# Kernel optimization log

Measured on AMD Instinct MI355X. Metric: run time of the kernel, lower is better.

## Reference

```python
import jax, jax.numpy as jnp
import numpy as np

N_NODES = 100000
N_EDGES = 1600000
N_FEAT = 128
HIDDEN = 128
N_GRAPHS = 1024


def setup_inputs() -> dict:
    key = jax.random.key(0)
    ks = jax.random.split(key, 9)
    x = jax.random.normal(ks[0], (N_NODES, N_FEAT), dtype=jnp.float32)
    edge_index = jax.random.randint(ks[1], (2, N_EDGES), 0, N_NODES, dtype=jnp.int64)
    batch = jnp.sort(jax.random.randint(ks[2], (N_NODES,), 0, N_GRAPHS, dtype=jnp.int64))
    W1 = jax.random.normal(ks[3], (N_FEAT, HIDDEN), dtype=jnp.float32) * (1.0 / np.sqrt(N_FEAT))
    b1 = jax.random.normal(ks[4], (HIDDEN,), dtype=jnp.float32) * 0.01
    W2 = jax.random.normal(ks[5], (HIDDEN, HIDDEN), dtype=jnp.float32) * (1.0 / np.sqrt(HIDDEN))
    b2 = jax.random.normal(ks[6], (HIDDEN,), dtype=jnp.float32) * 0.01
    Wl = jax.random.normal(ks[7], (HIDDEN, 2), dtype=jnp.float32) * (1.0 / np.sqrt(HIDDEN))
    bl = jax.random.normal(ks[8], (2,), dtype=jnp.float32) * 0.01
    return {"x": x, "edge_index": edge_index, "batch": batch,
            "W1": W1, "b1": b1, "W2": W2, "b2": b2, "Wl": Wl, "bl": bl}


def _gcn_norm(edge_index, num_nodes):
    # PyG GCNConv: add self-loops, then sym-normalize with in-degree (target col).
    loop = jnp.arange(num_nodes, dtype=edge_index.dtype)
    src = jnp.concatenate([edge_index[0], loop])  # [E+N]
    dst = jnp.concatenate([edge_index[1], loop])  # [E+N]
    deg = jax.ops.segment_sum(jnp.ones_like(dst, dtype=jnp.float32), dst,
                              num_segments=num_nodes)
    dinv = jnp.where(deg > 0, jax.lax.rsqrt(deg), 0.0)
    norm = dinv[src] * dinv[dst]  # [E+N]
    return src, dst, norm


def _gcn_conv(h, W, b, src, dst, norm, num_nodes):
    h = h @ W                                   # [N, out]
    msg = h[src] * norm[:, None]                # gather + scale, [E+N, out]
    agg = jax.ops.segment_sum(msg, dst, num_segments=num_nodes)  # scatter-add
    return agg + b


def reference(x, edge_index, batch, W1, b1, W2, b2, Wl, bl):
    n = x.shape[0]
    src, dst, norm = _gcn_norm(edge_index, n)
    h = jax.nn.relu(_gcn_conv(x, W1, b1, src, dst, norm, n))
    h = jax.nn.relu(_gcn_conv(h, W2, b2, src, dst, norm, n))
    # global_mean_pool over graph ids
    sums = jax.ops.segment_sum(h, batch, num_segments=N_GRAPHS)        # [G, H]
    counts = jax.ops.segment_sum(jnp.ones((n,), jnp.float32), batch,
                                 num_segments=N_GRAPHS)
    pooled = sums / jnp.maximum(counts, 1.0)[:, None]
    # F.dropout with training=False default in inference -> identity
    return pooled @ Wl + bl  # [G, 2]
```

## Files before the change

### kernel.cpp

```cpp
#include <hip/hip_runtime.h>
#include <hip/hip_bf16.h>

#define N_NODES 100000
#define N_EDGES 1600000
#define FEAT 128
#define N_GRAPHS 1024
#define NBUCK 391
#define CHUNK 4096

typedef short short8 __attribute__((ext_vector_type(8)));
typedef float float4v __attribute__((ext_vector_type(4)));

static __device__ inline unsigned short f2bf(float f) {
    __hip_bfloat16 b = __float2bfloat16(f);
    unsigned short r;
    __builtin_memcpy(&r, &b, 2);
    return r;
}
static __device__ inline float bf_lo(unsigned int v) { return __uint_as_float(v << 16); }
static __device__ inline float bf_hi(unsigned int v) { return __uint_as_float(v & 0xFFFF0000u); }

__global__ __launch_bounds__(256) void k_hist(const int* __restrict__ dst,
                                              int* __restrict__ bcount) {
    __shared__ int h[NBUCK];
    for (int i = threadIdx.x; i < NBUCK; i += 256) h[i] = 0;
    __syncthreads();
    for (int e = blockIdx.x * 256 + threadIdx.x; e < N_EDGES; e += gridDim.x * 256)
        atomicAdd(&h[dst[e] >> 8], 1);
    __syncthreads();
    for (int i = threadIdx.x; i < NBUCK; i += 256) {
        int c = h[i];
        if (c) atomicAdd(&bcount[i], c);
    }
}

__global__ __launch_bounds__(512) void k_scan391(const int* __restrict__ in,
                                                 int* __restrict__ base,
                                                 int* __restrict__ cur,
                                                 int* __restrict__ tail) {
    int t = threadIdx.x;
    int v = (t < NBUCK) ? in[t] : 0;
    int lane = t & 63, wid = t >> 6;
    int s = v;
#pragma unroll
    for (int d = 1; d < 64; d <<= 1) { int n = __shfl_up(s, d); if (lane >= d) s += n; }
    __shared__ int ws[8];
    if (lane == 63) ws[wid] = s;
    __syncthreads();
    if (t < 8) {
        int x = ws[t];
#pragma unroll
        for (int d = 1; d < 8; d <<= 1) { int n = __shfl_up(x, d); if ((int)t >= d) x += n; }
        ws[t] = x;
    }
    __syncthreads();
    int excl = s - v + (wid ? ws[wid - 1] : 0);
    if (t < NBUCK) {
        base[t] = excl;
        if (cur) cur[t] = excl;
    }
    if (t == 0 && tail) tail[0] = N_EDGES;
}

__global__ __launch_bounds__(256) void k_bucket(const int* __restrict__ src,
                                                const int* __restrict__ dst,
                                                int* __restrict__ bcur,
                                                uint2* __restrict__ pairs) {
    __shared__ int cnt[NBUCK];
    __shared__ int basebuf[NBUCK];
    int t = threadIdx.x;
    int e0 = blockIdx.x * CHUNK;
    for (int i = t; i < NBUCK; i += 256) cnt[i] = 0;
    __syncthreads();
    int es[16], ed[16];
#pragma unroll
    for (int j = 0; j < 16; ++j) {
        int e = e0 + j * 256 + t;
        if (e < N_EDGES) {
            es[j] = src[e];
            ed[j] = dst[e];
            atomicAdd(&cnt[ed[j] >> 8], 1);
        } else ed[j] = -1;
    }
    __syncthreads();
    for (int i = t; i < NBUCK; i += 256) {
        int c = cnt[i];
        basebuf[i] = c ? atomicAdd(&bcur[i], c) : 0;
        cnt[i] = 0;
    }
    __syncthreads();
#pragma unroll
    for (int j = 0; j < 16; ++j) {
        if (ed[j] >= 0) {
            int b = ed[j] >> 8;
            int p = basebuf[b] + atomicAdd(&cnt[b], 1);
            pairs[p] = make_uint2((unsigned)es[j], (unsigned)ed[j]);
        }
    }
}

__global__ __launch_bounds__(256) void k_bdeg(const uint2* __restrict__ pairs,
                                              const int* __restrict__ bbase,
                                              const int* __restrict__ bcount,
                                              int* __restrict__ deg,
                                              float* __restrict__ dinv,
                                              int* __restrict__ wsum) {
    __shared__ int d[256];
    __shared__ int wr[4];
    int b = blockIdx.x, t = threadIdx.x;
    d[t] = 0;
    __syncthreads();
    int s0 = bbase[b], n = bcount[b];
    for (int i = t; i < n; i += 256) atomicAdd(&d[pairs[s0 + i].y & 255], 1);
    __syncthreads();
    int node = b * 256 + t;
    int v = d[t];
    if (node < N_NODES) {
        deg[node] = v;
        dinv[node] = rsqrtf((float)(v + 1));
    }
#pragma unroll
    for (int dd = 32; dd > 0; dd >>= 1) v += __shfl_down(v, dd);
    if ((t & 63) == 0) wr[t >> 6] = v;
    __syncthreads();
    if (t == 0) wsum[b] = wr[0] + wr[1] + wr[2] + wr[3];
}

__global__ __launch_bounds__(256) void k_bfill(const uint2* __restrict__ pairs,
                                               const int* __restrict__ bbase,
                                               const int* __restrict__ bcount,
                                               const int* __restrict__ deg,
                                               const int* __restrict__ wbase,
                                               int* __restrict__ offs,
                                               int* __restrict__ csr) {
    __shared__ int lcur[256];
    __shared__ int ws[4];
    int b = blockIdx.x, t = threadIdx.x;
    int node = b * 256 + t;
    int dv = (node < N_NODES) ? deg[node] : 0;
    int lane = t & 63, wid = t >> 6;
    int s = dv;
#pragma unroll
    for (int d = 1; d < 64; d <<= 1) { int n = __shfl_up(s, d); if (lane >= d) s += n; }
    if (lane == 63) ws[wid] = s;
    __syncthreads();
    if (t < 4) {
        int x = ws[t];
#pragma unroll
        for (int d = 1; d < 4; d <<= 1) { int n = __shfl_up(x, d); if ((int)t >= d) x += n; }
        ws[t] = x;
    }
    __syncthreads();
    int excl = s - dv + (wid ? ws[wid - 1] : 0) + wbase[b];
    if (node < N_NODES) offs[node] = excl;
    lcur[t] = excl;
    __syncthreads();
    int s0 = bbase[b], n = bcount[b];
    for (int i = t; i < n; i += 256) {
        uint2 pr = pairs[s0 + i];
        int p = atomicAdd(&lcur[pr.y & 255], 1);
        csr[p] = (int)pr.x;
    }
}

__global__ __launch_bounds__(256) void k_prepW(const float* __restrict__ W,
                                               unsigned short* __restrict__ wp) {
    int t = blockIdx.x * 256 + threadIdx.x;
    if (t >= 16384) return;
    int k = t >> 7, n = t & 127;
    float w = W[k * 128 + n];
    unsigned ub = __float_as_uint(w);
    unsigned short hi = (unsigned short)(ub >> 16);
    float hif = __uint_as_float(ub & 0xFFFF0000u);
    unsigned short lo = f2bf(w - hif);
    int sidx = n * 128 + ((k & 7) | (8 * (((k >> 3) ^ n) & 15)));
    wp[sidx] = hi;
    wp[16384 + sidx] = lo;
}

__global__ __launch_bounds__(256) void k_gemm_mfma(const float* __restrict__ inp,
                                                   const unsigned short* __restrict__ wp,
                                                   const float* __restrict__ dinv,
                                                   unsigned short* __restrict__ u) {
    __shared__ unsigned short sW[32768];
    {
        float4* d4 = (float4*)sW;
        const float4* s4 = (const float4*)wp;
#pragma unroll
        for (int i = 0; i < 16; ++i) d4[threadIdx.x + 256 * i] = s4[threadIdx.x + 256 * i];
    }
    __syncthreads();
    const int t = threadIdx.x;
    const int wv = t >> 6, L = t & 63;
    const int m = L & 15, q = L >> 4;
    const int r0 = blockIdx.x * 64 + wv * 16;
    int arow = r0 + m;
    if (arow >= N_NODES) arow = N_NODES - 1;
    const float4* ap = (const float4*)(inp + (size_t)arow * 128);
    float4v acc[8];
#pragma unroll
    for (int c = 0; c < 8; ++c) acc[c] = (float4v){0.f, 0.f, 0.f, 0.f};

#pragma unroll
    for (int k0 = 0; k0 < 128; k0 += 32) {
        float4 f0 = ap[(k0 >> 2) + 2 * q];
        float4 f1 = ap[(k0 >> 2) + 2 * q + 1];
        float fa[8] = {f0.x, f0.y, f0.z, f0.w, f1.x, f1.y, f1.z, f1.w};
        short8 ah, al;
#pragma unroll
        for (int j = 0; j < 8; ++j) {
            unsigned ub = __float_as_uint(fa[j]);
            ah[j] = (short)(ub >> 16);
            float hif = __uint_as_float(ub & 0xFFFF0000u);
            al[j] = (short)f2bf(fa[j] - hif);
        }
        const int b = (k0 >> 3) + q;
#pragma unroll
        for (int c = 0; c < 8; ++c) {
            int ng = c * 16 + m;
            int elem = ng * 128 + 8 * ((b ^ ng) & 15);
            short8 bh = *(const short8*)&sW[elem];
            short8 bl = *(const short8*)&sW[16384 + elem];
            acc[c] = __builtin_amdgcn_mfma_f32_16x16x32_bf16(ah, bh, acc[c], 0, 0, 0);
            acc[c] = __builtin_amdgcn_mfma_f32_16x16x32_bf16(al, bh, acc[c], 0, 0, 0);
            acc[c] = __builtin_amdgcn_mfma_f32_16x16x32_bf16(ah, bl, acc[c], 0, 0, 0);
        }
    }
#pragma unroll
    for (int r = 0; r < 4; ++r) {
        int row = r0 + 4 * q + r;
        if (row < N_NODES) {
            float dv = dinv[row];
            unsigned short* up = u + (size_t)row * 128 + m;
#pragma unroll
            for (int c = 0; c < 8; ++c) up[c * 16] = f2bf(dv * acc[c][r]);
        }
    }
}

__global__ __launch_bounds__(256) void k_agg(const unsigned int* __restrict__ u,
                                             const int* __restrict__ offs,
                                             const int* __restrict__ csr,
                                             const float* __restrict__ dinv,
                                             const float* __restrict__ bias,
                                             float* __restrict__ hout) {
    int wid = threadIdx.x >> 6;
    int lane = threadIdx.x & 63;
    int node = __builtin_amdgcn_readfirstlane(blockIdx.x * 4 + wid);
    if (node >= N_NODES) return;
    int p = __builtin_amdgcn_readfirstlane(offs[node]);
    int e = __builtin_amdgcn_readfirstlane(offs[node + 1]);
    unsigned int self = u[(size_t)node * 64 + lane];
    float ax0 = bf_lo(self), ay0 = bf_hi(self);
    float ax1 = 0.f, ay1 = 0.f, ax2 = 0.f, ay2 = 0.f, ax3 = 0.f, ay3 = 0.f;
    float ax4 = 0.f, ay4 = 0.f, ax5 = 0.f, ay5 = 0.f, ax6 = 0.f, ay6 = 0.f;
    float ax7 = 0.f, ay7 = 0.f;
    for (; p < e; p += 8) {
        int c0 = csr[p + 0], c1 = csr[p + 1], c2 = csr[p + 2], c3 = csr[p + 3];
        int c4 = csr[p + 4], c5 = csr[p + 5], c6 = csr[p + 6], c7 = csr[p + 7];
        int i0 = c0;
        int i1 = (p + 1 < e) ? c1 : N_NODES;
        int i2 = (p + 2 < e) ? c2 : N_NODES;
        int i3 = (p + 3 < e) ? c3 : N_NODES;
        int i4 = (p + 4 < e) ? c4 : N_NODES;
        int i5 = (p + 5 < e) ? c5 : N_NODES;
        int i6 = (p + 6 < e) ? c6 : N_NODES;
        int i7 = (p + 7 < e) ? c7 : N_NODES;
        unsigned v0 = (u + (size_t)i0 * 64)[lane];
        unsigned v1 = (u + (size_t)i1 * 64)[lane];
        unsigned v2 = (u + (size_t)i2 * 64)[lane];
        unsigned v3 = (u + (size_t)i3 * 64)[lane];
        unsigned v4 = (u + (size_t)i4 * 64)[lane];
        unsigned v5 = (u + (size_t)i5 * 64)[lane];
        unsigned v6 = (u + (size_t)i6 * 64)[lane];
        unsigned v7 = (u + (size_t)i7 * 64)[lane];
        ax0 += bf_lo(v0); ay0 += bf_hi(v0);
        ax1 += bf_lo(v1); ay1 += bf_hi(v1);
        ax2 += bf_lo(v2); ay2 += bf_hi(v2);
        ax3 += bf_lo(v3); ay3 += bf_hi(v3);
        ax4 += bf_lo(v4); ay4 += bf_hi(v4);
        ax5 += bf_lo(v5); ay5 += bf_hi(v5);
        ax6 += bf_lo(v6); ay6 += bf_hi(v6);
        ax7 += bf_lo(v7); ay7 += bf_hi(v7);
    }
    float d = dinv[node];
    float2 b = ((const float2*)bias)[lane];
    float sx = ((ax0 + ax1) + (ax2 + ax3)) + ((ax4 + ax5) + (ax6 + ax7));
    float sy = ((ay0 + ay1) + (ay2 + ay3)) + ((ay4 + ay5) + (ay6 + ay7));
    float r0 = fmaxf(d * sx + b.x, 0.f);
    float r1 = fmaxf(d * sy + b.y, 0.f);
    ((float2*)hout)[(size_t)node * 64 + lane] = make_float2(r0, r1);
}

__global__ __launch_bounds__(128) void k_pool(const float* __restrict__ h,
                                              const int* __restrict__ batch,
                                              const float* __restrict__ Wl,
                                              const float* __restrict__ bl,
                                              float* __restrict__ out) {
    int g = blockIdx.x;
    int c = threadIdx.x;
    __shared__ int sb[2];
    if (c < 2) {
        int tgt = g + c;
        int lo = 0, hi = N_NODES;
        while (lo < hi) { int m = (lo + hi) >> 1; if (batch[m] < tgt) lo = m + 1; else hi = m; }
        sb[c] = lo;
    }
    __syncthreads();
    int s0 = sb[0], s1 = sb[1];
    float sum = 0.f;
    for (int i = s0; i < s1; ++i) sum += h[(size_t)i * 128 + c];
    float cnt = (float)(s1 - s0);
    float pooled = sum / fmaxf(cnt, 1.0f);
    __shared__ float red[128];
    float w0 = Wl[c * 2 + 0], w1 = Wl[c * 2 + 1];
    red[c] = pooled * w0;
    __syncthreads();
    for (int st = 64; st > 0; st >>= 1) { if (c < st) red[c] += red[c + st]; __syncthreads(); }
    if (c == 0) out[g * 2 + 0] = red[0] + bl[0];
    __syncthreads();
    red[c] = pooled * w1;
    __syncthreads();
    for (int st = 64; st > 0; st >>= 1) { if (c < st) red[c] += red[c + st]; __syncthreads(); }
    if (c == 0) out[g * 2 + 1] = red[0] + bl[1];
}

extern "C" void kernel_launch(void* const* d_in, const int* in_sizes, int n_in,
                              void* d_out, int out_size, void* d_ws, size_t ws_size,
                              hipStream_t stream) {
    const float* x  = (const float*)d_in[0];
    const int* ei   = (const int*)d_in[1];
    const int* batch = (const int*)d_in[2];
    const float* W1 = (const float*)d_in[3];
    const float* b1 = (const float*)d_in[4];
    const float* W2 = (const float*)d_in[5];
    const float* b2 = (const float*)d_in[6];
    const float* Wl = (const float*)d_in[7];
    const float* bl = (const float*)d_in[8];
    float* out = (float*)d_out;
    const int* src = ei;
    const int* dst = ei + N_EDGES;

    char* ws = (char*)d_ws;
    size_t o = 0;
    auto alloc = [&](size_t bytes) -> void* {
        o = (o + 255) & ~(size_t)255;
        void* p = ws + o;
        o += bytes;
        return p;
    };
    int* bcount = (int*)alloc((size_t)NBUCK * 4);
    int* bbase  = (int*)alloc((size_t)NBUCK * 4);
    int* bcur   = (int*)alloc((size_t)NBUCK * 4);
    int* wsum   = (int*)alloc((size_t)NBUCK * 4);
    int* wbase  = (int*)alloc((size_t)NBUCK * 4);
    int* deg    = (int*)alloc((size_t)N_NODES * 4);
    float* dinv = (float*)alloc((size_t)N_NODES * 4);
    int* offs   = (int*)alloc((size_t)(N_NODES + 1) * 4);
    unsigned short* wp1 = (unsigned short*)alloc(65536);
    unsigned short* wp2 = (unsigned short*)alloc(65536);
    uint2* pairs = (uint2*)alloc((size_t)N_EDGES * 8);
    int* csr    = (int*)alloc((size_t)(N_EDGES + 8) * 4);
    unsigned short* u = (unsigned short*)alloc((size_t)(N_NODES + 1) * 128 * 2);
    float* h    = (float*)alloc((size_t)N_NODES * 128 * 4);

    hipMemsetAsync(bcount, 0, (size_t)NBUCK * 4, stream);
    hipMemsetAsync(u + (size_t)N_NODES * 128, 0, 256, stream);
    k_prepW<<<64, 256, 0, stream>>>(W1, wp1);
    k_prepW<<<64, 256, 0, stream>>>(W2, wp2);
    k_hist<<<256, 256, 0, stream>>>(dst, bcount);
    k_scan391<<<1, 512, 0, stream>>>(bcount, bbase, bcur, nullptr);
    k_bucket<<<(N_EDGES + CHUNK - 1) / CHUNK, 256, 0, stream>>>(src, dst, bcur, pairs);
    k_bdeg<<<NBUCK, 256, 0, stream>>>(pairs, bbase, bcount, deg, dinv, wsum);
    k_scan391<<<1, 512, 0, stream>>>(wsum, wbase, nullptr, &offs[N_NODES]);
    k_bfill<<<NBUCK, 256, 0, stream>>>(pairs, bbase, bcount, deg, wbase, offs, csr);

    const int gemmGrid = (N_NODES + 63) / 64;
    k_gemm_mfma<<<gemmGrid, 256, 0, stream>>>(x, wp1, dinv, u);
    k_agg<<<(N_NODES + 3) / 4, 256, 0, stream>>>((const unsigned int*)u, offs, csr, dinv, b1, h);
    k_gemm_mfma<<<gemmGrid, 256, 0, stream>>>(h, wp2, dinv, u);
    k_agg<<<(N_NODES + 3) / 4, 256, 0, stream>>>((const unsigned int*)u, offs, csr, dinv, b2, h);

    k_pool<<<N_GRAPHS, 128, 0, stream>>>(h, batch, Wl, bl, out);
}
```

Before: 375.2 us.

## Store hidden activations as split bf16 hi/lo, pack edge pairs, fuse prep kernels

The aggregation kernel now writes its output as two bf16 planes (hi and residual lo) in place of fp32. A new GEMM variant feeds these planes straight into MFMA without converting fp32 to bf16 itself, and pooling sums hi+lo. Edge bucket pairs are packed into one 32-bit word (src<<8 | dst&255), halving that intermediate traffic. The two weight-prep kernels and the memsets are merged into one launch. Total bytes moved stay about the same for h, but the GEMM's conversion work and launch overhead go down. Packing src<<8 relies on node ids fitting in 24 bits.

```diff
diff --git a/kernel.cpp b/kernel.cpp
--- a/kernel.cpp
+++ b/kernel.cpp
@@ -19,6 +19,32 @@
 }
 static __device__ inline float bf_lo(unsigned int v) { return __uint_as_float(v << 16); }
 static __device__ inline float bf_hi(unsigned int v) { return __uint_as_float(v & 0xFFFF0000u); }
+static __device__ inline float bf_s(unsigned short s) { return __uint_as_float(((unsigned)s) << 16); }
+
+__global__ __launch_bounds__(256) void k_prep(const float* __restrict__ W1,
+                                              const float* __restrict__ W2,
+                                              unsigned short* __restrict__ wp1,
+                                              unsigned short* __restrict__ wp2,
+                                              int* __restrict__ bcount,
+                                              unsigned int* __restrict__ udummy) {
+    int bid = blockIdx.x;
+    const float* W = (bid < 64) ? W1 : W2;
+    unsigned short* wp = (bid < 64) ? wp1 : wp2;
+    int t = (bid & 63) * 256 + threadIdx.x;
+    int k = t >> 7, n = t & 127;
+    float w = W[k * 128 + n];
+    unsigned ub = __float_as_uint(w);
+    unsigned short hi = (unsigned short)(ub >> 16);
+    float hif = __uint_as_float(ub & 0xFFFF0000u);
+    unsigned short lo = f2bf(w - hif);
+    int sidx = n * 128 + ((k & 7) | (8 * (((k >> 3) ^ n) & 15)));
+    wp[sidx] = hi;
+    wp[16384 + sidx] = lo;
+    if (bid == 0) {
+        for (int i = threadIdx.x; i < NBUCK; i += 256) bcount[i] = 0;
+        if (threadIdx.x < 64) udummy[threadIdx.x] = 0;
+    }
+}
 
 __global__ __launch_bounds__(256) void k_hist(const int* __restrict__ dst,
                                               int* __restrict__ bcount) {
@@ -65,22 +91,23 @@
 __global__ __launch_bounds__(256) void k_bucket(const int* __restrict__ src,
                                                 const int* __restrict__ dst,
                                                 int* __restrict__ bcur,
-                                                uint2* __restrict__ pairs) {
+                                                unsigned int* __restrict__ pairs) {
     __shared__ int cnt[NBUCK];
     __shared__ int basebuf[NBUCK];
     int t = threadIdx.x;
     int e0 = blockIdx.x * CHUNK;
     for (int i = t; i < NBUCK; i += 256) cnt[i] = 0;
     __syncthreads();
-    int es[16], ed[16];
+    unsigned pk[16]; int bk[16];
 #pragma unroll
     for (int j = 0; j < 16; ++j) {
         int e = e0 + j * 256 + t;
         if (e < N_EDGES) {
-            es[j] = src[e];
-            ed[j] = dst[e];
-            atomicAdd(&cnt[ed[j] >> 8], 1);
-        } else ed[j] = -1;
+            int s = src[e], d = dst[e];
+            bk[j] = d >> 8;
+            pk[j] = ((unsigned)s << 8) | (unsigned)(d & 255);
+            atomicAdd(&cnt[bk[j]], 1);
+        } else bk[j] = -1;
     }
     __syncthreads();
     for (int i = t; i < NBUCK; i += 256) {
@@ -91,15 +118,14 @@
     __syncthreads();
 #pragma unroll
     for (int j = 0; j < 16; ++j) {
-        if (ed[j] >= 0) {
-            int b = ed[j] >> 8;
-            int p = basebuf[b] + atomicAdd(&cnt[b], 1);
-            pairs[p] = make_uint2((unsigned)es[j], (unsigned)ed[j]);
-        }
-    }
-}
-
-__global__ __launch_bounds__(256) void k_bdeg(const uint2* __restrict__ pairs,
+        if (bk[j] >= 0) {
+            int p = basebuf[bk[j]] + atomicAdd(&cnt[bk[j]], 1);
+            pairs[p] = pk[j];
+        }
+    }
+}
+
+__global__ __launch_bounds__(256) void k_bdeg(const unsigned int* __restrict__ pairs,
                                               const int* __restrict__ bbase,
                                               const int* __restrict__ bcount,
                                               int* __restrict__ deg,
@@ -111,7 +137,7 @@
     d[t] = 0;
     __syncthreads();
     int s0 = bbase[b], n = bcount[b];
-    for (int i = t; i < n; i += 256) atomicAdd(&d[pairs[s0 + i].y & 255], 1);
+    for (int i = t; i < n; i += 256) atomicAdd(&d[pairs[s0 + i] & 255u], 1);
     __syncthreads();
     int node = b * 256 + t;
     int v = d[t];
@@ -126,7 +152,7 @@
     if (t == 0) wsum[b] = wr[0] + wr[1] + wr[2] + wr[3];
 }
 
-__global__ __launch_bounds__(256) void k_bfill(const uint2* __restrict__ pairs,
+__global__ __launch_bounds__(256) void k_bfill(const unsigned int* __restrict__ pairs,
                                                const int* __restrict__ bbase,
                                                const int* __restrict__ bcount,
                                                const int* __restrict__ deg,
@@ -157,25 +183,10 @@
     __syncthreads();
     int s0 = bbase[b], n = bcount[b];
     for (int i = t; i < n; i += 256) {
-        uint2 pr = pairs[s0 + i];
-        int p = atomicAdd(&lcur[pr.y & 255], 1);
-        csr[p] = (int)pr.x;
-    }
-}
-
-__global__ __launch_bounds__(256) void k_prepW(const float* __restrict__ W,
-                                               unsigned short* __restrict__ wp) {
-    int t = blockIdx.x * 256 + threadIdx.x;
-    if (t >= 16384) return;
-    int k = t >> 7, n = t & 127;
-    float w = W[k * 128 + n];
-    unsigned ub = __float_as_uint(w);
-    unsigned short hi = (unsigned short)(ub >> 16);
-    float hif = __uint_as_float(ub & 0xFFFF0000u);
-    unsigned short lo = f2bf(w - hif);
-    int sidx = n * 128 + ((k & 7) | (8 * (((k >> 3) ^ n) & 15)));
-    wp[sidx] = hi;
-    wp[16384 + sidx] = lo;
+        unsigned pr = pairs[s0 + i];
+        int p = atomicAdd(&lcur[pr & 255u], 1);
+        csr[p] = (int)(pr >> 8);
+    }
 }
 
 __global__ __launch_bounds__(256) void k_gemm_mfma(const float* __restrict__ inp,
@@ -238,12 +249,66 @@
     }
 }
 
+__global__ __launch_bounds__(256) void k_gemm_mfma_bf(const unsigned short* __restrict__ hh,
+                                                      const unsigned short* __restrict__ hl,
+                                                      const unsigned short* __restrict__ wp,
+                                                      const float* __restrict__ dinv,
+                                                      unsigned short* __restrict__ u) {
+    __shared__ unsigned short sW[32768];
+    {
+        float4* d4 = (float4*)sW;
+        const float4* s4 = (const float4*)wp;
+#pragma unroll
+        for (int i = 0; i < 16; ++i) d4[threadIdx.x + 256 * i] = s4[threadIdx.x + 256 * i];
+    }
+    __syncthreads();
+    const int t = threadIdx.x;
+    const int wv = t >> 6, L = t & 63;
+    const int m = L & 15, q = L >> 4;
+    const int r0 = blockIdx.x * 64 + wv * 16;
+    int arow = r0 + m;
+    if (arow >= N_NODES) arow = N_NODES - 1;
+    const unsigned short* hhp = hh + (size_t)arow * 128 + 8 * q;
+    const unsigned short* hlp = hl + (size_t)arow * 128 + 8 * q;
+    float4v acc[8];
+#pragma unroll
+    for (int c = 0; c < 8; ++c) acc[c] = (float4v){0.f, 0.f, 0.f, 0.f};
+
+#pragma unroll
+    for (int k0 = 0; k0 < 128; k0 += 32) {
+        short8 ah = *(const short8*)(hhp + k0);
+        short8 al = *(const short8*)(hlp + k0);
+        const int b = (k0 >> 3) + q;
+#pragma unroll
+        for (int c = 0; c < 8; ++c) {
+            int ng = c * 16 + m;
+            int elem = ng * 128 + 8 * ((b ^ ng) & 15);
+            short8 bh = *(const short8*)&sW[elem];
+            short8 bl = *(const short8*)&sW[16384 + elem];
+            acc[c] = __builtin_amdgcn_mfma_f32_16x16x32_bf16(ah, bh, acc[c], 0, 0, 0);
+            acc[c] = __builtin_amdgcn_mfma_f32_16x16x32_bf16(al, bh, acc[c], 0, 0, 0);
+            acc[c] = __builtin_amdgcn_mfma_f32_16x16x32_bf16(ah, bl, acc[c], 0, 0, 0);
+        }
+    }
+#pragma unroll
+    for (int r = 0; r < 4; ++r) {
+        int row = r0 + 4 * q + r;
+        if (row < N_NODES) {
+            float dv = dinv[row];
+            unsigned short* up = u + (size_t)row * 128 + m;
+#pragma unroll
+            for (int c = 0; c < 8; ++c) up[c * 16] = f2bf(dv * acc[c][r]);
+        }
+    }
+}
+
 __global__ __launch_bounds__(256) void k_agg(const unsigned int* __restrict__ u,
                                              const int* __restrict__ offs,
                                              const int* __restrict__ csr,
                                              const float* __restrict__ dinv,
                                              const float* __restrict__ bias,
-                                             float* __restrict__ hout) {
+                                             unsigned int* __restrict__ hhp,
+                                             unsigned int* __restrict__ hlp) {
     int wid = threadIdx.x >> 6;
     int lane = threadIdx.x & 63;
     int node = __builtin_amdgcn_readfirstlane(blockIdx.x * 4 + wid);
@@ -289,10 +354,16 @@
     float sy = ((ay0 + ay1) + (ay2 + ay3)) + ((ay4 + ay5) + (ay6 + ay7));
     float r0 = fmaxf(d * sx + b.x, 0.f);
     float r1 = fmaxf(d * sy + b.y, 0.f);
-    ((float2*)hout)[(size_t)node * 64 + lane] = make_float2(r0, r1);
-}
-
-__global__ __launch_bounds__(128) void k_pool(const float* __restrict__ h,
+    unsigned u0 = __float_as_uint(r0), u1 = __float_as_uint(r1);
+    unsigned short h0 = (unsigned short)(u0 >> 16), h1 = (unsigned short)(u1 >> 16);
+    float rf0 = __uint_as_float(u0 & 0xFFFF0000u), rf1 = __uint_as_float(u1 & 0xFFFF0000u);
+    unsigned short l0 = f2bf(r0 - rf0), l1 = f2bf(r1 - rf1);
+    hhp[(size_t)node * 64 + lane] = (unsigned)h0 | ((unsigned)h1 << 16);
+    hlp[(size_t)node * 64 + lane] = (unsigned)l0 | ((unsigned)l1 << 16);
+}
+
+__global__ __launch_bounds__(128) void k_pool(const unsigned short* __restrict__ hh,
+                                              const unsigned short* __restrict__ hl,
                                               const int* __restrict__ batch,
                                               const float* __restrict__ Wl,
                                               const float* __restrict__ bl,
@@ -309,7 +380,10 @@
     __syncthreads();
     int s0 = sb[0], s1 = sb[1];
     float sum = 0.f;
-    for (int i = s0; i < s1; ++i) sum += h[(size_t)i * 128 + c];
+    for (int i = s0; i < s1; ++i) {
+        float v = bf_s(hh[(size_t)i * 128 + c]) + bf_s(hl[(size_t)i * 128 + c]);
+        sum += v;
+    }
     float cnt = (float)(s1 - s0);
     float pooled = sum / fmaxf(cnt, 1.0f);
     __shared__ float red[128];
@@ -359,15 +433,14 @@
     int* offs   = (int*)alloc((size_t)(N_NODES + 1) * 4);
     unsigned short* wp1 = (unsigned short*)alloc(65536);
     unsigned short* wp2 = (unsigned short*)alloc(65536);
-    uint2* pairs = (uint2*)alloc((size_t)N_EDGES * 8);
+    unsigned int* pairs = (unsigned int*)alloc((size_t)N_EDGES * 4);
     int* csr    = (int*)alloc((size_t)(N_EDGES + 8) * 4);
     unsigned short* u = (unsigned short*)alloc((size_t)(N_NODES + 1) * 128 * 2);
-    float* h    = (float*)alloc((size_t)N_NODES * 128 * 4);
-
-    hipMemsetAsync(bcount, 0, (size_t)NBUCK * 4, stream);
-    hipMemsetAsync(u + (size_t)N_NODES * 128, 0, 256, stream);
-    k_prepW<<<64, 256, 0, stream>>>(W1, wp1);
-    k_prepW<<<64, 256, 0, stream>>>(W2, wp2);
+    unsigned short* hh = (unsigned short*)alloc((size_t)N_NODES * 128 * 2);
+    unsigned short* hl = (unsigned short*)alloc((size_t)N_NODES * 128 * 2);
+
+    k_prep<<<128, 256, 0, stream>>>(W1, W2, wp1, wp2, bcount,
+                                    (unsigned int*)(u + (size_t)N_NODES * 128));
     k_hist<<<256, 256, 0, stream>>>(dst, bcount);
     k_scan391<<<1, 512, 0, stream>>>(bcount, bbase, bcur, nullptr);
     k_bucket<<<(N_EDGES + CHUNK - 1) / CHUNK, 256, 0, stream>>>(src, dst, bcur, pairs);
@@ -377,9 +450,11 @@
 
     const int gemmGrid = (N_NODES + 63) / 64;
     k_gemm_mfma<<<gemmGrid, 256, 0, stream>>>(x, wp1, dinv, u);
-    k_agg<<<(N_NODES + 3) / 4, 256, 0, stream>>>((const unsigned int*)u, offs, csr, dinv, b1, h);
-    k_gemm_mfma<<<gemmGrid, 256, 0, stream>>>(h, wp2, dinv, u);
-    k_agg<<<(N_NODES + 3) / 4, 256, 0, stream>>>((const unsigned int*)u, offs, csr, dinv, b2, h);
-
-    k_pool<<<N_GRAPHS, 128, 0, stream>>>(h, batch, Wl, bl, out);
-}
+    k_agg<<<(N_NODES + 3) / 4, 256, 0, stream>>>((const unsigned int*)u, offs, csr, dinv, b1,
+                                                 (unsigned int*)hh, (unsigned int*)hl);
+    k_gemm_mfma_bf<<<gemmGrid, 256, 0, stream>>>(hh, hl, wp2, dinv, u);
+    k_agg<<<(N_NODES + 3) / 4, 256, 0, stream>>>((const unsigned int*)u, offs, csr, dinv, b2,
+                                                 (unsigned int*)hh, (unsigned int*)hl);
+
+    k_pool<<<N_GRAPHS, 128, 0, stream>>>(hh, hl, batch, Wl, bl, out);
+}
```

Result: faster. 366.5 us (-2.3%).
